# Kernel tuning notes

Hardware: AMD Instinct MI355X
Metric: run time of the kernel (lower is better)

Reference implementation:

```python
import jax, jax.numpy as jnp
import numpy as np

# Static hyperparams matching init_kwargs
KSIZE, STRIDE, PAD, DIL = 3, 2, 1, 1


def setup_inputs() -> dict:
    key = jax.random.key(0)
    k1, k2 = jax.random.split(key)
    B, H, W, Cin, Cout = 8, 128, 128, 128, 256
    feats = jax.random.normal(k1, (B * H * W, Cin), dtype=jnp.float32)
    weight = jax.random.normal(k2, (KSIZE * KSIZE, Cin, Cout), dtype=jnp.float32) * 0.05
    alpha_upper = jnp.ones((1,), dtype=jnp.float32)
    # dense grid coords [N, 3] = (batch, y, x), matching a dense image sparse tensor
    bb, yy, xx = np.meshgrid(np.arange(B), np.arange(H), np.arange(W), indexing='ij')
    coords = jnp.asarray(np.stack([bb, yy, xx], -1).reshape(-1, 3), dtype=jnp.int32)
    return {"feats": feats, "weight": weight, "alpha_upper": alpha_upper,
            "coords": coords, "H": H, "W": W, "B": B}


def _coord_ranges(H, W):
    # Faithful translation of WrappedMinkowskiStridedOperation.__init__ + forward
    # coordinate math, specialized to a dense grid (per-batch min=0, max=H-1/W-1).
    kernel_origin = DIL * ((KSIZE - 1) // 2) * (KSIZE % 2)
    dilated = DIL * (KSIZE - 1) + 1
    ks_off = kernel_origin - dilated + 1          # _kernel_start_offset
    ke_off = kernel_origin                        # _kernel_end_offset
    idx_start = kernel_origin - PAD               # _index_start_offset
    ranges = []
    for ext in (H, W):
        idx_end = (ext - 1) + kernel_origin + PAD - dilated + 2
        start = max(idx_start, (0 + ks_off - idx_start) // STRIDE * STRIDE + idx_start)
        end = min(idx_end, ((ext - 1 + ke_off - idx_start) // STRIDE + 1) * STRIDE + idx_start)
        ranges.append(np.arange(start, end, STRIDE))
    offsets = np.arange(KSIZE) * DIL - kernel_origin  # kernel region offsets
    return ranges[0], ranges[1], offsets, idx_start


def reference(feats, weight, alpha_upper, coords, H, W, B):
    Cin = feats.shape[1]
    Cout = weight.shape[-1]
    ys, xs, offs, idx_start = _coord_ranges(H, W)
    OH, OW = len(ys), len(xs)
    oy, ox = jnp.meshgrid(jnp.asarray(ys, jnp.int32), jnp.asarray(xs, jnp.int32), indexing='ij')
    dy, dx = np.meshgrid(offs, offs, indexing='ij')
    dy = jnp.asarray(dy.reshape(-1), jnp.int32)  # [kvol]
    dx = jnp.asarray(dx.reshape(-1), jnp.int32)
    ny = oy[None] + dy[:, None, None]            # [kvol, OH, OW]
    nx = ox[None] + dx[:, None, None]
    valid = (ny >= 0) & (ny < H) & (nx >= 0) & (nx < W)
    lin = jnp.clip(ny, 0, H - 1) * W + jnp.clip(nx, 0, W - 1)  # [kvol, OH, OW]
    feats3 = feats.reshape(B, H * W, Cin)
    gathered = feats3[:, lin]                    # [B, kvol, OH, OW, Cin]
    gathered = jnp.where(valid[None, ..., None], gathered, jnp.zeros((), feats.dtype))
    out = jnp.einsum('bkhwc,kcd->bhwd', gathered, weight)  # [B, OH, OW, Cout]
    out_feats = out.reshape(B * OH * OW, Cout)
    # output coordinates, remapped as in forward (shift by index_start, divide by stride)
    oc = jnp.stack([oy, ox], -1).reshape(-1, 2)  # [OH*OW, 2]
    oc = (oc - jnp.int32(idx_start)) // jnp.int32(STRIDE)
    oc = jnp.tile(oc, (B, 1))
    bcol = jnp.repeat(jnp.arange(B, dtype=jnp.int32), OH * OW)
    out_coords = jnp.concatenate([bcol[:, None], oc], axis=1)
    return out_feats, out_coords, alpha_upper
```

## Files before the change

### kernel.cpp

```cpp
#include <hip/hip_runtime.h>


#define OUT_FEATS_ELEMS (32768 * 256)
#define OUT_COORDS_OFF  OUT_FEATS_ELEMS
#define ALPHA_OFF       (OUT_FEATS_ELEMS + 32768 * 3)

#define BW_BYTES   (18 * 16384)

typedef float v16f __attribute__((ext_vector_type(16)));

__device__ __forceinline__ unsigned pk4fp8(float a, float b, float c, float d) {
    unsigned u = 0;
    u = __builtin_amdgcn_cvt_pk_fp8_f32(a, b, u, false);
    u = __builtin_amdgcn_cvt_pk_fp8_f32(c, d, u, true);
    return u;
}

#define GLOAD_LDS16(SRC, DST)                                                  \
    __builtin_amdgcn_global_load_lds(                                          \
        (const __attribute__((address_space(1))) void*)(SRC),                  \
        (__attribute__((address_space(3))) void*)(DST), 16, 0, 0)

#define WAITBAR_(N) asm volatile("s_waitcnt vmcnt(" #N ")\n\ts_barrier" ::: "memory")
#define WAITBAR(N)  WAITBAR_(N)
#define BAR()       asm volatile("s_barrier" ::: "memory")
#define LGKMBAR()   asm volatile("s_waitcnt lgkmcnt(0)\n\ts_barrier" ::: "memory")

__global__ void wprep_kernel(const float* __restrict__ w,
                             const float* __restrict__ alpha,
                             unsigned char* __restrict__ Bw,
                             float* __restrict__ out) {
    int cid = blockIdx.x * 256 + threadIdx.x;
    if (cid < 32768) {
        int b = cid >> 12, iy = (cid >> 6) & 63, ix = cid & 63;
        float* c = out + OUT_COORDS_OFF + (size_t)cid * 3;
        c[0] = (float)b; c[1] = (float)iy; c[2] = (float)ix;
        if (cid == 0) out[ALPHA_OFF] = alpha[0];
    }
    if (cid < 18432) {
        int ch  = cid & 7;
        int row = (cid >> 3) & 127;
        int t   = cid >> 10;
        int nb  = (t >= 9) ? 1 : 0;
        int tap = t - 9 * nb;
        int chp = ch ^ (row & 7);
        int hb  = (row >> 3) & 1;
        int n   = (nb << 7) + row;
        int kb  = (tap << 7) + (chp << 4);
        unsigned u[4];
#pragma unroll
        for (int q = 0; q < 4; ++q) {
            int kq = kb + 4 * (q ^ (hb << 1));
            float f0 = w[(size_t)(kq + 0) * 256 + n];
            float f1 = w[(size_t)(kq + 1) * 256 + n];
            float f2 = w[(size_t)(kq + 2) * 256 + n];
            float f3 = w[(size_t)(kq + 3) * 256 + n];
            u[q] = pk4fp8(f0, f1, f2, f3);
        }
        uint4 r; r.x = u[0]; r.y = u[1]; r.z = u[2]; r.w = u[3];
        *(uint4*)(Bw + (size_t)cid * 16) = r;
    }
}

__global__ void coords_alpha_kernel(float* __restrict__ out, const float* __restrict__ alpha) {
    int i = blockIdx.x * 256 + threadIdx.x;
    int b = i >> 12, iy = (i >> 6) & 63, ix = i & 63;
    float* c = out + OUT_COORDS_OFF + (size_t)i * 3;
    c[0] = (float)b; c[1] = (float)iy; c[2] = (float)ix;
    if (i == 0) out[ALPHA_OFF] = alpha[0];
}

__global__ __launch_bounds__(512, 1) void gemm_conv_kernel(
    const float* __restrict__ feats,
    const unsigned char* __restrict__ Bw,
    float* __restrict__ out)
{
    __shared__ unsigned char Aband[5 * 130 * 128];
    __shared__ unsigned char Bs[2][256 * 128];

    const int tid  = threadIdx.x;
    const int bid  = blockIdx.x;
    const int my   = ((bid & 7) << 5) + (bid >> 3);
    const int m0   = my << 7;
    const int bb   = my >> 5;
    const int iy0  = ((my & 31) << 1);

    const int lane = tid & 63, wave = tid >> 6;
    const int wm   = (wave >> 2) << 6;
    const int wn   = (wave & 3) << 6;
    const int l31  = lane & 31;
    const int hh   = lane >> 5;
    const int xorl = l31 & 7;
    const int bhalf = (hh ^ ((l31 >> 3) & 1)) << 3;

    const unsigned char* bsrc0 = Bw + ((size_t)((wave >> 2) * 9) << 14)
                                    + ((size_t)(wave & 3) << 12) + ((size_t)lane << 4);
    auto stageB = [&](int tap, int buf) {
        const unsigned char* bs = bsrc0 + ((size_t)tap << 14);
        unsigned char* bdst = Bs[buf] + (wave << 12);
#pragma unroll
        for (int q = 0; q < 4; ++q)
            GLOAD_LDS16(bs + (q << 10), bdst + (q << 10));
    };

    const int ny0 = (iy0 << 1) - 1;
    auto issueRow = [&](int r, float4* f) {
        const int ny = ny0 + r;
#pragma unroll
        for (int it = 0; it < 8; ++it) {
            const int idx = (it << 9) + tid;
            const int nx  = idx >> 5;
            const int c4  = (idx & 31) << 2;
            f[it] = *(const float4*)(feats +
                ((((size_t)(bb << 14) + ny * 128 + nx)) << 7) + c4);
        }
    };
    auto writeRow = [&](int r, const float4* f) {
#pragma unroll
        for (int it = 0; it < 8; ++it) {
            const int idx = (it << 9) + tid;
            const int nx  = idx >> 5;
            const int c4  = (idx & 31) << 2;
            const unsigned u = pk4fp8(f[it].x, f[it].y, f[it].z, f[it].w);
            const int nxp  = nx + 1;
            const int key4 = (nxp >> 1) & 15;
            const int boff = ((r * 130 + nxp) << 7)
                + (((c4 >> 4) ^ (key4 & 7)) << 4)
                + (((((c4 >> 3) & 1) ^ (key4 >> 3)) & 1) << 3)
                + (c4 & 7);
            *(unsigned*)(Aband + boff) = u;
        }
    };

    stageB(0, 0);
    if (tid < 40) {
        const int r = tid >> 3, c = tid & 7;
        uint4 z; z.x = 0u; z.y = 0u; z.z = 0u; z.w = 0u;
        *(uint4*)(Aband + ((r * 130) << 7) + (c << 4)) = z;
    }
    if (iy0 == 0) {
        for (int z = tid; z < 1040; z += 512) {
            uint4 zz; zz.x = 0u; zz.y = 0u; zz.z = 0u; zz.w = 0u;
            *(uint4*)(Aband + z * 16) = zz;
        }
    }
    float4 fA[8], fB[8];
    if (iy0 > 0) issueRow(0, fA);
    issueRow(2, fB);
    if (iy0 > 0) writeRow(0, fA);
    writeRow(2, fB);
    __syncthreads();

    v16f acc[2][2];
#pragma unroll
    for (int i = 0; i < 2; i++)
#pragma unroll
        for (int j = 0; j < 2; j++) acc[i][j] = (v16f)(0.0f);

    auto computeTap = [&](int buf, int dy, int dx) {
        const int bandrow = (wm >> 5) + dy + 1;
        int abase[2], kc[2];
#pragma unroll
        for (int i = 0; i < 2; ++i) {
            const int ixv  = (i << 5) + l31;
            const int nxp  = (ixv << 1) + dx + 1;
            const int key4 = (nxp >> 1) & 15;
            abase[i] = ((bandrow * 130 + nxp) << 7) + ((hh ^ (key4 >> 3)) << 3);
            kc[i]    = key4 & 7;
        }
#pragma unroll
        for (int seg = 0; seg < 8; ++seg) {
            long long a[2], b2[2];
#pragma unroll
            for (int i = 0; i < 2; i++)
                a[i] = *(const long long*)(Aband + abase[i] + ((seg ^ kc[i]) << 4));
#pragma unroll
            for (int j = 0; j < 2; j++)
                b2[j] = *(const long long*)(Bs[buf] + ((wn + (j << 5) + l31) << 7)
                                            + ((seg ^ xorl) << 4) + bhalf);
            __builtin_amdgcn_s_setprio(1);
#pragma unroll
            for (int i = 0; i < 2; i++)
#pragma unroll
                for (int j = 0; j < 2; j++)
                    acc[i][j] = __builtin_amdgcn_mfma_f32_32x32x16_fp8_fp8(a[i], b2[j], acc[i][j], 0, 0, 0);
            __builtin_amdgcn_s_setprio(0);
        }
    };

    stageB(1, 1); issueRow(1, fA); issueRow(3, fB);
    BAR();
    computeTap(0, -1, -1); BAR();
    stageB(2, 0); WAITBAR(20);
    computeTap(1, -1, 0); BAR();
    stageB(3, 1); WAITBAR(4);
    computeTap(0, -1, 1);
    writeRow(1, fA); writeRow(3, fB);
    LGKMBAR();
    stageB(4, 0); issueRow(4, fA); WAITBAR(12);
    computeTap(1, 0, -1); BAR();
    stageB(5, 1); WAITBAR(12);
    computeTap(0, 0, 0); BAR();
    stageB(6, 0); WAITBAR(4);
    computeTap(1, 0, 1);
    writeRow(4, fA);
    LGKMBAR();
    stageB(7, 1); WAITBAR(4);
    computeTap(0, 1, -1); BAR();
    stageB(8, 0); WAITBAR(4);
    computeTap(1, 1, 0); BAR();
    WAITBAR(0);
    computeTap(0, 1, 1);

#pragma unroll
    for (int i = 0; i < 2; i++)
#pragma unroll
        for (int j = 0; j < 2; j++) {
            const int gcol = wn + (j << 5) + l31;
#pragma unroll
            for (int r = 0; r < 16; ++r) {
                const int grow = m0 + wm + (i << 5) + (r & 3) + ((r >> 2) << 3) + (hh << 2);
                __builtin_nontemporal_store(acc[i][j][r], &out[(size_t)grow * 256 + gcol]);
            }
        }
}

__global__ void naive_conv_kernel(const float* __restrict__ feats,
                                  const float* __restrict__ w,
                                  float* __restrict__ out) {
    int m = blockIdx.x;
    int n = threadIdx.x;
    int bb = m >> 12, iy = (m >> 6) & 63, ix = m & 63;
    float acc = 0.f;
    for (int tap = 0; tap < 9; ++tap) {
        int ny = 2 * iy + tap / 3 - 1;
        int nx = 2 * ix + tap % 3 - 1;
        if ((unsigned)ny < 128u && (unsigned)nx < 128u) {
            const float* fr = feats + ((size_t)((bb << 14) + (ny << 7) + nx) << 7);
            const float* wr = w + tap * 32768 + n;
            for (int c = 0; c < 128; ++c) acc += fr[c] * wr[c * 256];
        }
    }
    out[(size_t)m * 256 + n] = acc;
}

extern "C" void kernel_launch(void* const* d_in, const int* in_sizes, int n_in,
                              void* d_out, int out_size, void* d_ws, size_t ws_size,
                              hipStream_t stream) {
    const float* feats  = (const float*)d_in[0];
    const float* weight = (const float*)d_in[1];
    const float* alpha  = (const float*)d_in[2];
    float* out = (float*)d_out;

    const size_t NEED = (size_t)BW_BYTES;
    if (ws_size >= NEED) {
        unsigned char* Bw = (unsigned char*)d_ws;
        wprep_kernel<<<144, 256, 0, stream>>>(weight, alpha, Bw, out);
        gemm_conv_kernel<<<256, 512, 0, stream>>>(feats, Bw, out);
    } else {
        coords_alpha_kernel<<<128, 256, 0, stream>>>(out, alpha);
        naive_conv_kernel<<<32768, 256, 0, stream>>>(feats, weight, out);
    }
}
```

Baseline: 128.1 us.

## Halve per-block tile to one output row, single-buffer weights, raise occupancy

Each block now computes one output row of 64 pixels instead of two. The A band shrinks to 3 input rows with no padding column, and the left pad is handled by zeroing the A operand in registers. The weight buffer becomes single-buffered and the hand-scheduled software pipeline is replaced by a simple loop of compute, barrier, load next tap, wait. Smaller LDS and register use permit multiple blocks per CU with twice as many blocks, relying on occupancy to hide latency, but per-block pipelining is lost and each block does half the MFMAs per B load.

```diff
diff --git a/kernel.cpp b/kernel.cpp
--- a/kernel.cpp
+++ b/kernel.cpp
@@ -24,7 +24,6 @@
 #define WAITBAR_(N) asm volatile("s_waitcnt vmcnt(" #N ")\n\ts_barrier" ::: "memory")
 #define WAITBAR(N)  WAITBAR_(N)
 #define BAR()       asm volatile("s_barrier" ::: "memory")
-#define LGKMBAR()   asm volatile("s_waitcnt lgkmcnt(0)\n\ts_barrier" ::: "memory")
 
 __global__ void wprep_kernel(const float* __restrict__ w,
                              const float* __restrict__ alpha,
@@ -70,23 +69,23 @@
     if (i == 0) out[ALPHA_OFF] = alpha[0];
 }
 
-__global__ __launch_bounds__(512, 1) void gemm_conv_kernel(
+__global__ __launch_bounds__(512, 4) void gemm_conv_kernel(
     const float* __restrict__ feats,
     const unsigned char* __restrict__ Bw,
     float* __restrict__ out)
 {
-    __shared__ unsigned char Aband[5 * 130 * 128];
-    __shared__ unsigned char Bs[2][256 * 128];
+    __shared__ unsigned char Aband[3 * 128 * 128];
+    __shared__ unsigned char Bs[256 * 128];
 
     const int tid  = threadIdx.x;
     const int bid  = blockIdx.x;
-    const int my   = ((bid & 7) << 5) + (bid >> 3);
-    const int m0   = my << 7;
-    const int bb   = my >> 5;
-    const int iy0  = ((my & 31) << 1);
+    const int my   = ((bid & 7) << 6) + ((bid >> 3) & 63);
+    const int m0   = my << 6;
+    const int bb   = my >> 6;
+    const int iy   = my & 63;
 
     const int lane = tid & 63, wave = tid >> 6;
-    const int wm   = (wave >> 2) << 6;
+    const int wm   = (wave >> 2) << 5;
     const int wn   = (wave & 3) << 6;
     const int l31  = lane & 31;
     const int hh   = lane >> 5;
@@ -95,15 +94,17 @@
 
     const unsigned char* bsrc0 = Bw + ((size_t)((wave >> 2) * 9) << 14)
                                     + ((size_t)(wave & 3) << 12) + ((size_t)lane << 4);
-    auto stageB = [&](int tap, int buf) {
+    auto stageB = [&](int tap) {
         const unsigned char* bs = bsrc0 + ((size_t)tap << 14);
-        unsigned char* bdst = Bs[buf] + (wave << 12);
+        unsigned char* bdst = Bs + (wave << 12);
 #pragma unroll
         for (int q = 0; q < 4; ++q)
             GLOAD_LDS16(bs + (q << 10), bdst + (q << 10));
     };
 
-    const int ny0 = (iy0 << 1) - 1;
+    stageB(0);
+
+    const int ny0 = (iy << 1) - 1;
     auto issueRow = [&](int r, float4* f) {
         const int ny = ny0 + r;
 #pragma unroll
@@ -122,9 +123,8 @@
             const int nx  = idx >> 5;
             const int c4  = (idx & 31) << 2;
             const unsigned u = pk4fp8(f[it].x, f[it].y, f[it].z, f[it].w);
-            const int nxp  = nx + 1;
-            const int key4 = (nxp >> 1) & 15;
-            const int boff = ((r * 130 + nxp) << 7)
+            const int key4 = ((nx + 1) >> 1) & 15;
+            const int boff = ((r * 128 + nx) << 7)
                 + (((c4 >> 4) ^ (key4 & 7)) << 4)
                 + (((((c4 >> 3) & 1) ^ (key4 >> 3)) & 1) << 3)
                 + (c4 & 7);
@@ -132,97 +132,74 @@
         }
     };
 
-    stageB(0, 0);
-    if (tid < 40) {
-        const int r = tid >> 3, c = tid & 7;
-        uint4 z; z.x = 0u; z.y = 0u; z.z = 0u; z.w = 0u;
-        *(uint4*)(Aband + ((r * 130) << 7) + (c << 4)) = z;
-    }
-    if (iy0 == 0) {
-        for (int z = tid; z < 1040; z += 512) {
+    if (iy == 0) {
+        for (int z = tid; z < 1024; z += 512) {
             uint4 zz; zz.x = 0u; zz.y = 0u; zz.z = 0u; zz.w = 0u;
             *(uint4*)(Aband + z * 16) = zz;
         }
     }
-    float4 fA[8], fB[8];
-    if (iy0 > 0) issueRow(0, fA);
-    issueRow(2, fB);
-    if (iy0 > 0) writeRow(0, fA);
-    writeRow(2, fB);
+    {
+        float4 fA[8], fB[8];
+        const int r0 = (iy == 0) ? 1 : 0;
+        issueRow(r0, fA);
+        issueRow(r0 + 1, fB);
+        writeRow(r0, fA);
+        issueRow(2, fA);
+        writeRow(r0 + 1, fB);
+        if (r0 + 1 != 2) writeRow(2, fA);
+        else {  writeRow(2, fA); }
+    }
     __syncthreads();
 
-    v16f acc[2][2];
-#pragma unroll
-    for (int i = 0; i < 2; i++)
-#pragma unroll
-        for (int j = 0; j < 2; j++) acc[i][j] = (v16f)(0.0f);
-
-    auto computeTap = [&](int buf, int dy, int dx) {
-        const int bandrow = (wm >> 5) + dy + 1;
-        int abase[2], kc[2];
-#pragma unroll
-        for (int i = 0; i < 2; ++i) {
-            const int ixv  = (i << 5) + l31;
-            const int nxp  = (ixv << 1) + dx + 1;
-            const int key4 = (nxp >> 1) & 15;
-            abase[i] = ((bandrow * 130 + nxp) << 7) + ((hh ^ (key4 >> 3)) << 3);
-            kc[i]    = key4 & 7;
-        }
+    v16f acc[2];
+#pragma unroll
+    for (int j = 0; j < 2; j++) acc[j] = (v16f)(0.0f);
+
+    auto computeTap = [&](int dy, int dx) {
+        const int r   = dy + 1;
+        const int ixv = wm + l31;
+        const int nxq = (ixv << 1) + dx;
+        const bool pad = (nxq < 0);
+        const int nxs = pad ? 0 : nxq;
+        const int key4 = ((nxq + 1) >> 1) & 15;
+        const int abase = ((r * 128 + nxs) << 7) + ((hh ^ (key4 >> 3)) << 3);
+        const int kc = key4 & 7;
 #pragma unroll
         for (int seg = 0; seg < 8; ++seg) {
-            long long a[2], b2[2];
-#pragma unroll
-            for (int i = 0; i < 2; i++)
-                a[i] = *(const long long*)(Aband + abase[i] + ((seg ^ kc[i]) << 4));
+            long long a0 = *(const long long*)(Aband + abase + ((seg ^ kc) << 4));
+            if (pad) a0 = 0LL;
+            long long b2[2];
 #pragma unroll
             for (int j = 0; j < 2; j++)
-                b2[j] = *(const long long*)(Bs[buf] + ((wn + (j << 5) + l31) << 7)
+                b2[j] = *(const long long*)(Bs + ((wn + (j << 5) + l31) << 7)
                                             + ((seg ^ xorl) << 4) + bhalf);
             __builtin_amdgcn_s_setprio(1);
 #pragma unroll
-            for (int i = 0; i < 2; i++)
-#pragma unroll
-                for (int j = 0; j < 2; j++)
-                    acc[i][j] = __builtin_amdgcn_mfma_f32_32x32x16_fp8_fp8(a[i], b2[j], acc[i][j], 0, 0, 0);
+            for (int j = 0; j < 2; j++)
+                acc[j] = __builtin_amdgcn_mfma_f32_32x32x16_fp8_fp8(a0, b2[j], acc[j], 0, 0, 0);
             __builtin_amdgcn_s_setprio(0);
         }
     };
 
-    stageB(1, 1); issueRow(1, fA); issueRow(3, fB);
-    BAR();
-    computeTap(0, -1, -1); BAR();
-    stageB(2, 0); WAITBAR(20);
-    computeTap(1, -1, 0); BAR();
-    stageB(3, 1); WAITBAR(4);
-    computeTap(0, -1, 1);
-    writeRow(1, fA); writeRow(3, fB);
-    LGKMBAR();
-    stageB(4, 0); issueRow(4, fA); WAITBAR(12);
-    computeTap(1, 0, -1); BAR();
-    stageB(5, 1); WAITBAR(12);
-    computeTap(0, 0, 0); BAR();
-    stageB(6, 0); WAITBAR(4);
-    computeTap(1, 0, 1);
-    writeRow(4, fA);
-    LGKMBAR();
-    stageB(7, 1); WAITBAR(4);
-    computeTap(0, 1, -1); BAR();
-    stageB(8, 0); WAITBAR(4);
-    computeTap(1, 1, 0); BAR();
-    WAITBAR(0);
-    computeTap(0, 1, 1);
-
-#pragma unroll
-    for (int i = 0; i < 2; i++)
-#pragma unroll
-        for (int j = 0; j < 2; j++) {
-            const int gcol = wn + (j << 5) + l31;
-#pragma unroll
-            for (int r = 0; r < 16; ++r) {
-                const int grow = m0 + wm + (i << 5) + (r & 3) + ((r >> 2) << 3) + (hh << 2);
-                __builtin_nontemporal_store(acc[i][j][r], &out[(size_t)grow * 256 + gcol]);
-            }
-        }
+#pragma unroll
+    for (int tap = 0; tap < 9; ++tap) {
+        computeTap(tap / 3 - 1, tap % 3 - 1);
+        if (tap < 8) {
+            BAR();
+            stageB(tap + 1);
+            WAITBAR(0);
+        }
+    }
+
+#pragma unroll
+    for (int j = 0; j < 2; j++) {
+        const int gcol = wn + (j << 5) + l31;
+#pragma unroll
+        for (int r = 0; r < 16; ++r) {
+            const int grow = m0 + wm + (r & 3) + ((r >> 2) << 3) + (hh << 2);
+            __builtin_nontemporal_store(acc[j][r], &out[(size_t)grow * 256 + gcol]);
+        }
+    }
 }
 
 __global__ void naive_conv_kernel(const float* __restrict__ feats,
@@ -256,7 +233,7 @@
     if (ws_size >= NEED) {
         unsigned char* Bw = (unsigned char*)d_ws;
         wprep_kernel<<<144, 256, 0, stream>>>(weight, alpha, Bw, out);
-        gemm_conv_kernel<<<256, 512, 0, stream>>>(feats, Bw, out);
+        gemm_conv_kernel<<<512, 512, 0, stream>>>(feats, Bw, out);
     } else {
         coords_alpha_kernel<<<128, 256, 0, stream>>>(out, alpha);
         naive_conv_kernel<<<32768, 256, 0, stream>>>(feats, weight, out);
```

Measured after the change: 128.3 us. No clear change (+0.1%).
